# Kernel tuning notes

Measured on AMD Instinct MI355X. Metric: run time of the kernel, lower is better.

The kernel has to match this reference:

```python
import jax, jax.numpy as jnp
import numpy as np

B, T, D, H, L = 64, 512, 1024, 1024, 4


def setup_inputs() -> dict:
    key = jax.random.key(0)
    ks = jax.random.split(key, 5)
    scale = 1.0 / np.sqrt(H)
    return {
        "x": jax.random.normal(ks[0], (B, T, D), dtype=jnp.float32),
        "Wih": jax.random.normal(ks[1], (L, 4 * H, D), dtype=jnp.float32) * scale,
        "Whh": jax.random.normal(ks[2], (L, 4 * H, H), dtype=jnp.float32) * scale,
        "bih": jax.random.normal(ks[3], (L, 4 * H), dtype=jnp.float32) * scale,
        "bhh": jax.random.normal(ks[4], (L, 4 * H), dtype=jnp.float32) * scale,
    }


def _lstm_layer(x_tbd, Wih, Whh, b):
    # x_tbd: [T, B, in]; Wih: [4H, in]; Whh: [4H, H]; b: [4H]
    Bsz = x_tbd.shape[1]
    Hsz = Whh.shape[1]
    # precompute the input-side GEMM for the whole sequence in one shot
    xg = jnp.einsum('tbd,gd->tbg', x_tbd, Wih) + b  # [T, B, 4H]

    def step(carry, xg_t):
        h, c = carry
        z = xg_t + h @ Whh.T  # [B, 4H]
        i, f, g, o = jnp.split(z, 4, axis=-1)  # torch LSTMCell gate order
        c = jax.nn.sigmoid(f) * c + jax.nn.sigmoid(i) * jnp.tanh(g)
        h = jax.nn.sigmoid(o) * jnp.tanh(c)
        return (h, c), h

    init = (jnp.zeros((Bsz, Hsz), x_tbd.dtype), jnp.zeros((Bsz, Hsz), x_tbd.dtype))
    (h_last, _), hs = jax.lax.scan(step, init, xg)
    return hs, h_last  # hs: [T, B, H]


def reference(x, Wih, Whh, bih, bhh):
    # layer-by-layer over the stack (fixed small L); each layer scans over time
    seq = jnp.transpose(x, (1, 0, 2))  # [T, B, D]
    h_last = None
    for l in range(L):
        seq, h_last = _lstm_layer(seq, Wih[l], Whh[l], bih[l] + bhh[l])
    return h_last  # [B, output_size], hidden of last layer at final timestep
```

## Files before the change

### kernel.cpp

```cpp
#include <hip/hip_runtime.h>
#include <math.h>


#define BSZ 64
#define TSZ 512
#define DSZ 1024
#define HSZ 1024
#define LSZ 4
#define NBLK 256
#define NTHR 512
#define NSTEP (TSZ + LSZ - 1)
#define BUFB 32768

typedef _Float16 half8  __attribute__((ext_vector_type(8)));
typedef _Float16 half4  __attribute__((ext_vector_type(4)));
typedef _Float16 half2v __attribute__((ext_vector_type(2)));
typedef float    f32x4  __attribute__((ext_vector_type(4)));
typedef float    f32x8  __attribute__((ext_vector_type(8)));

constexpr size_t N_X  = (size_t)BSZ * TSZ * DSZ;
constexpr size_t N_H  = (size_t)2 * LSZ * BSZ * HSZ;
constexpr size_t OFF_X     = 0;
constexpr size_t OFF_H     = OFF_X + N_X * 2;
constexpr size_t OFF_FLAGS = OFF_H + N_H * 2;
constexpr size_t OFF_GEN   = OFF_FLAGS + (size_t)NBLK * 64;
constexpr size_t BAR_BYTES = (size_t)NBLK * 64 + 64;

__device__ inline float fsig(float x) {
  return __builtin_amdgcn_rcpf(1.0f + __expf(-x));
}
__device__ inline float ftanh(float x) {
  float e = __expf(fminf(2.0f * x, 80.0f));
  return 1.0f - 2.0f * __builtin_amdgcn_rcpf(e + 1.0f);
}

__device__ inline void gload16(const void* g, void* l) {
  __builtin_amdgcn_global_load_lds(
      (const __attribute__((address_space(1))) void*)g,
      (__attribute__((address_space(3))) void*)l, 16, 0, 0);
}

__device__ inline void gbar(unsigned* flags, unsigned* gen, unsigned tgt) {
  __syncthreads();
  if (blockIdx.x == 0) {
    const int t = threadIdx.x;
    if (t >= 1 && t < NBLK) {
      while (__hip_atomic_load(&flags[t * 16], __ATOMIC_RELAXED,
                               __HIP_MEMORY_SCOPE_AGENT) < tgt)
        __builtin_amdgcn_s_sleep(2);
    }
    __syncthreads();
    if (t == 0) {
      __hip_atomic_store(gen, tgt, __ATOMIC_RELAXED, __HIP_MEMORY_SCOPE_AGENT);
      __builtin_amdgcn_fence(__ATOMIC_ACQUIRE, "agent");
    }
  } else {
    if (threadIdx.x == 0) {
      __hip_atomic_store(&flags[(size_t)blockIdx.x * 16], tgt, __ATOMIC_RELAXED,
                         __HIP_MEMORY_SCOPE_AGENT);
      while (__hip_atomic_load(gen, __ATOMIC_RELAXED,
                               __HIP_MEMORY_SCOPE_AGENT) < tgt)
        __builtin_amdgcn_s_sleep(2);
      __builtin_amdgcn_fence(__ATOMIC_ACQUIRE, "agent");
    }
  }
  __syncthreads();
}

__global__ __launch_bounds__(NTHR, 1) void lstm_persistent(
    const float* __restrict__ xin, const float* __restrict__ Wih,
    const float* __restrict__ Whh, const float* __restrict__ bih,
    const float* __restrict__ bhh, float* __restrict__ out,
    char* __restrict__ ws)
{
  _Float16* x16   = (_Float16*)(ws + OFF_X);
  _Float16* h16   = (_Float16*)(ws + OFF_H);
  unsigned* flags = (unsigned*)(ws + OFF_FLAGS);
  unsigned* gen   = (unsigned*)(ws + OFF_GEN);

  const int tid  = threadIdx.x;
  const int gtid = blockIdx.x * NTHR + tid;
  const int lane = tid & 63;
  const int w    = tid >> 6;
  const int mat  = w >> 2;
  const int rp   = (w >> 1) & 1;
  const int kh   = w & 1;
  const int ln15 = lane & 15;
  const int lq   = lane >> 4;

  const int l  = blockIdx.x >> 6;
  const int cc = blockIdx.x & 63;
  const int c0 = cc * 16;

  const float* Wsel = mat ? Whh : Wih;
  half8 bw[2][16];
#pragma unroll
  for (int gl = 0; gl < 2; ++gl) {
    const float* wrow =
        Wsel + (size_t)(l * 4096 + (rp * 2 + gl) * 1024 + c0 + ln15) * 1024 +
        kh * 512;
#pragma unroll
    for (int ks = 0; ks < 16; ++ks) {
      f32x8 f = *(const f32x8*)(wrow + ks * 32 + lq * 8);
      bw[gl][ks] = __builtin_convertvector(f, half8);
    }
  }

  const int gb = tid >> 3;
  const int gc = (tid & 7) * 2;
  float bsg[4][2];
#pragma unroll
  for (int g = 0; g < 4; ++g) {
    const int bb = l * 4096 + g * 1024 + c0 + gc;
    bsg[g][0] = bih[bb] + bhh[bb];
    bsg[g][1] = bih[bb + 1] + bhh[bb + 1];
  }
  float cr0 = 0.f, cr1 = 0.f;

  const int sb   = tid >> 3;
  const int pswl = ((tid & 7) ^ (sb & 7)) << 4;
  const int dstb = (tid >> 6) << 10;

  {
    const f32x4* s4 = (const f32x4*)xin;
    unsigned long long* xu = (unsigned long long*)x16;
    const int dq = DSZ / 4;
    for (int i = gtid; i < (int)(N_X / 4); i += NBLK * NTHR) {
      const int d4  = i & (dq - 1);
      const int rem = i >> 8;
      const int tt  = rem & (TSZ - 1);
      const int bb  = rem >> 9;
      half4 v = __builtin_convertvector(s4[i], half4);
      const size_t o = ((size_t)tt * BSZ + bb) * dq + d4;
      __hip_atomic_store(&xu[o], __builtin_bit_cast(unsigned long long, v),
                         __ATOMIC_RELAXED, __HIP_MEMORY_SCOPE_AGENT);
    }
    unsigned long long* hz = (unsigned long long*)h16;
    for (int i = gtid; i < (int)(N_H / 4); i += NBLK * NTHR)
      __hip_atomic_store(&hz[i], 0ull, __ATOMIC_RELAXED,
                         __HIP_MEMORY_SCOPE_AGENT);
  }
  unsigned btgt = 1;
  gbar(flags, gen, btgt++);

  __shared__ __align__(16) char smem[3 * BUFB];
  float* pl = (float*)smem;

  const int lm1 = (l > 0) ? (l - 1) : 0;

  for (int s = 0; s < NSTEP; ++s) {
    const int t = s - l;
    if (t >= 0 && t < TSZ) {
      const int prevslot = (s + 1) & 1;
      const _Float16* hin  = h16 + (size_t)prevslot * (LSZ * BSZ * HSZ) +
                             (size_t)lm1 * (BSZ * HSZ);
      const _Float16* hown = h16 + (size_t)prevslot * (LSZ * BSZ * HSZ) +
                             (size_t)l * (BSZ * HSZ);
      const _Float16* base0 = (l == 0) ? x16 + (size_t)t * (BSZ * DSZ) : hin;

      const char* p0 = (const char*)(base0 + (size_t)sb * 1024) + pswl;
      const char* p1 = (const char*)(hown + (size_t)sb * HSZ) + pswl;

      auto stage = [&](int kc, int bsel) {
        const char* r0 = p0 + kc * 128;
        const char* r1 = p1 + kc * 128;
        char* d = smem + bsel * BUFB + dstb;
        gload16(r0,        d);
        gload16(r0 + 1024, d + 8192);
        gload16(r1,        d + 16384);
        gload16(r1 + 1024, d + 24576);
      };

      f32x4 acc[4][2] = {};

      stage(0, 0);
      stage(1, 1);
      __builtin_amdgcn_sched_barrier(0);
      asm volatile("s_waitcnt vmcnt(4)" ::: "memory");
      __builtin_amdgcn_s_barrier();
      __builtin_amdgcn_sched_barrier(0);

      const int rdoff = mat * 16384 + kh * 8192;
#pragma unroll
      for (int kc = 0; kc < 8; ++kc) {
        if (kc + 2 < 8) stage(kc + 2, (kc + 2) % 3);
        const char* rdb = smem + (kc % 3) * BUFB + rdoff;
#pragma unroll
        for (int ksl = 0; ksl < 2; ++ksl) {
#pragma unroll
          for (int mt = 0; mt < 4; ++mt) {
            const int row = mt * 16 + ln15;
            const half8 a = *(const half8*)(rdb + row * 128 +
                                            ((ksl * 64 + lq * 16) ^
                                             ((row & 7) << 4)));
            acc[mt][0] = __builtin_amdgcn_mfma_f32_16x16x32_f16(
                a, bw[0][kc * 2 + ksl], acc[mt][0], 0, 0, 0);
            acc[mt][1] = __builtin_amdgcn_mfma_f32_16x16x32_f16(
                a, bw[1][kc * 2 + ksl], acc[mt][1], 0, 0, 0);
          }
        }
        __builtin_amdgcn_sched_barrier(0);
        if (kc <= 5)      asm volatile("s_waitcnt vmcnt(4)" ::: "memory");
        else if (kc == 6) asm volatile("s_waitcnt vmcnt(0)" ::: "memory");
        __builtin_amdgcn_s_barrier();
        __builtin_amdgcn_sched_barrier(0);
      }

      if (l == 0 && t + 1 < TSZ) {
        const char* xnext =
            (const char*)(x16 + (size_t)(t + 1) * (BSZ * DSZ)) +
            ((cc >> 3) & 7) * 16384;
        char* trash = smem + 2 * BUFB + dstb;
        gload16(xnext + tid * 16, trash);
        gload16(xnext + 8192 + tid * 16, trash);
      }

      {
        const int pbase = (mat * 2 + kh) * 4096;
#pragma unroll
        for (int mt = 0; mt < 4; ++mt)
#pragma unroll
          for (int gl = 0; gl < 2; ++gl) {
            const int v  = (rp * 2 + gl) * 16 + ln15;
            const int bp = (mt * 16 + lq * 4) ^ ((ln15 & 7) << 2);
            *(f32x4*)&pl[pbase + v * 64 + bp] = acc[mt][gl];
          }
      }
      __builtin_amdgcn_sched_barrier(0);
      asm volatile("s_waitcnt lgkmcnt(0)" ::: "memory");
      __builtin_amdgcn_s_barrier();
      __builtin_amdgcn_sched_barrier(0);

      {
        float z[4][2];
#pragma unroll
        for (int g = 0; g < 4; ++g)
#pragma unroll
          for (int j = 0; j < 2; ++j) {
            const int v  = g * 16 + gc + j;
            const int bp = gb ^ ((v & 7) << 2);
            z[g][j] = pl[0 * 4096 + v * 64 + bp] +
                      pl[1 * 4096 + v * 64 + bp] +
                      pl[2 * 4096 + v * 64 + bp] +
                      pl[3 * 4096 + v * 64 + bp] + bsg[g][j];
          }
        float cn0 = fsig(z[1][0]) * cr0 + fsig(z[0][0]) * ftanh(z[2][0]);
        float cn1 = fsig(z[1][1]) * cr1 + fsig(z[0][1]) * ftanh(z[2][1]);
        float hn0 = fsig(z[3][0]) * ftanh(cn0);
        float hn1 = fsig(z[3][1]) * ftanh(cn1);
        cr0 = cn0; cr1 = cn1;
        half2v hv; hv[0] = (_Float16)hn0; hv[1] = (_Float16)hn1;
        const size_t ho = (size_t)(s & 1) * (LSZ * BSZ * HSZ) +
                          (size_t)l * (BSZ * HSZ) + (size_t)gb * HSZ + c0 + gc;
        __hip_atomic_store((unsigned*)(h16 + ho),
                           __builtin_bit_cast(unsigned, hv),
                           __ATOMIC_RELAXED, __HIP_MEMORY_SCOPE_AGENT);
        if (l == LSZ - 1 && t == TSZ - 1) {
          out[(size_t)gb * HSZ + c0 + gc]     = hn0;
          out[(size_t)gb * HSZ + c0 + gc + 1] = hn1;
        }
      }
    }
    gbar(flags, gen, btgt++);
  }
}

extern "C" void kernel_launch(void* const* d_in, const int* in_sizes, int n_in,
                              void* d_out, int out_size, void* d_ws, size_t ws_size,
                              hipStream_t stream) {
  const float* x   = (const float*)d_in[0];
  const float* Wih = (const float*)d_in[1];
  const float* Whh = (const float*)d_in[2];
  const float* bih = (const float*)d_in[3];
  const float* bhh = (const float*)d_in[4];
  float* out = (float*)d_out;
  char*  ws  = (char*)d_ws;

  hipMemsetAsync(ws + OFF_FLAGS, 0, BAR_BYTES, stream);

  void* args[] = {(void*)&x, (void*)&Wih, (void*)&Whh, (void*)&bih,
                  (void*)&bhh, (void*)&out, (void*)&ws};
  hipLaunchCooperativeKernel((const void*)lstm_persistent, dim3(NBLK), dim3(NTHR),
                             args, 0, stream);
}
```

Baseline: 4.563 ms.

## Split K across four waves per matrix and drop x-prefetch warm loads

Each wave now covers all four gates but only a quarter of the K range, instead of two gates over half of K. Each A fragment loaded from LDS is then reused across four MFMAs rather than two, which halves LDS reads per MFMA. The cost is a larger partial-sum buffer: eight partials per output instead of four, so shared memory grows to four buffers and the reduction does more LDS reads. The speculative L2 warm-up loads of the next timestep's x for layer 0 are also removed.

Result: slower. 4.901 ms (+7.4%).

```diff
diff --git a/kernel.cpp b/kernel.cpp
--- a/kernel.cpp
+++ b/kernel.cpp
@@ -83,8 +83,7 @@
   const int lane = tid & 63;
   const int w    = tid >> 6;
   const int mat  = w >> 2;
-  const int rp   = (w >> 1) & 1;
-  const int kh   = w & 1;
+  const int kq   = w & 3;
   const int ln15 = lane & 15;
   const int lq   = lane >> 4;
 
@@ -93,16 +92,16 @@
   const int c0 = cc * 16;
 
   const float* Wsel = mat ? Whh : Wih;
-  half8 bw[2][16];
-#pragma unroll
-  for (int gl = 0; gl < 2; ++gl) {
+  half8 bw[4][8];
+#pragma unroll
+  for (int g = 0; g < 4; ++g) {
     const float* wrow =
-        Wsel + (size_t)(l * 4096 + (rp * 2 + gl) * 1024 + c0 + ln15) * 1024 +
-        kh * 512;
-#pragma unroll
-    for (int ks = 0; ks < 16; ++ks) {
-      f32x8 f = *(const f32x8*)(wrow + ks * 32 + lq * 8);
-      bw[gl][ks] = __builtin_convertvector(f, half8);
+        Wsel + (size_t)(l * 4096 + g * 1024 + c0 + ln15) * 1024 +
+        (kq >> 1) * 512 + (kq & 1) * 32 + lq * 8;
+#pragma unroll
+    for (int kc = 0; kc < 8; ++kc) {
+      f32x8 f = *(const f32x8*)(wrow + kc * 64);
+      bw[g][kc] = __builtin_convertvector(f, half8);
     }
   }
 
@@ -143,7 +142,7 @@
   unsigned btgt = 1;
   gbar(flags, gen, btgt++);
 
-  __shared__ __align__(16) char smem[3 * BUFB];
+  __shared__ __align__(16) char smem[4 * BUFB];
   float* pl = (float*)smem;
 
   const int lm1 = (l > 0) ? (l - 1) : 0;
@@ -171,7 +170,7 @@
         gload16(r1 + 1024, d + 24576);
       };
 
-      f32x4 acc[4][2] = {};
+      f32x4 acc[4][4] = {};
 
       stage(0, 0);
       stage(1, 1);
@@ -180,25 +179,25 @@
       __builtin_amdgcn_s_barrier();
       __builtin_amdgcn_sched_barrier(0);
 
-      const int rdoff = mat * 16384 + kh * 8192;
+      const int rdoff = mat * 16384 + (kq >> 1) * 8192;
+      const int rdo   = (kq & 1) * 64 + lq * 16;
 #pragma unroll
       for (int kc = 0; kc < 8; ++kc) {
         if (kc + 2 < 8) stage(kc + 2, (kc + 2) % 3);
         const char* rdb = smem + (kc % 3) * BUFB + rdoff;
-#pragma unroll
-        for (int ksl = 0; ksl < 2; ++ksl) {
-#pragma unroll
-          for (int mt = 0; mt < 4; ++mt) {
-            const int row = mt * 16 + ln15;
-            const half8 a = *(const half8*)(rdb + row * 128 +
-                                            ((ksl * 64 + lq * 16) ^
-                                             ((row & 7) << 4)));
-            acc[mt][0] = __builtin_amdgcn_mfma_f32_16x16x32_f16(
-                a, bw[0][kc * 2 + ksl], acc[mt][0], 0, 0, 0);
-            acc[mt][1] = __builtin_amdgcn_mfma_f32_16x16x32_f16(
-                a, bw[1][kc * 2 + ksl], acc[mt][1], 0, 0, 0);
-          }
+        half8 a[4];
+#pragma unroll
+        for (int mt = 0; mt < 4; ++mt) {
+          const int row = mt * 16 + ln15;
+          a[mt] = *(const half8*)(rdb + row * 128 +
+                                  (rdo ^ ((row & 7) << 4)));
         }
+#pragma unroll
+        for (int g = 0; g < 4; ++g)
+#pragma unroll
+          for (int mt = 0; mt < 4; ++mt)
+            acc[mt][g] = __builtin_amdgcn_mfma_f32_16x16x32_f16(
+                a[mt], bw[g][kc], acc[mt][g], 0, 0, 0);
         __builtin_amdgcn_sched_barrier(0);
         if (kc <= 5)      asm volatile("s_waitcnt vmcnt(4)" ::: "memory");
         else if (kc == 6) asm volatile("s_waitcnt vmcnt(0)" ::: "memory");
@@ -206,24 +205,15 @@
         __builtin_amdgcn_sched_barrier(0);
       }
 
-      if (l == 0 && t + 1 < TSZ) {
-        const char* xnext =
-            (const char*)(x16 + (size_t)(t + 1) * (BSZ * DSZ)) +
-            ((cc >> 3) & 7) * 16384;
-        char* trash = smem + 2 * BUFB + dstb;
-        gload16(xnext + tid * 16, trash);
-        gload16(xnext + 8192 + tid * 16, trash);
-      }
-
       {
-        const int pbase = (mat * 2 + kh) * 4096;
+        const int pbase = w * 4096;
 #pragma unroll
         for (int mt = 0; mt < 4; ++mt)
 #pragma unroll
-          for (int gl = 0; gl < 2; ++gl) {
-            const int v  = (rp * 2 + gl) * 16 + ln15;
+          for (int g = 0; g < 4; ++g) {
+            const int v  = g * 16 + ln15;
             const int bp = (mt * 16 + lq * 4) ^ ((ln15 & 7) << 2);
-            *(f32x4*)&pl[pbase + v * 64 + bp] = acc[mt][gl];
+            *(f32x4*)&pl[pbase + v * 64 + bp] = acc[mt][g];
           }
       }
       __builtin_amdgcn_sched_barrier(0);
@@ -239,10 +229,11 @@
           for (int j = 0; j < 2; ++j) {
             const int v  = g * 16 + gc + j;
             const int bp = gb ^ ((v & 7) << 2);
-            z[g][j] = pl[0 * 4096 + v * 64 + bp] +
-                      pl[1 * 4096 + v * 64 + bp] +
-                      pl[2 * 4096 + v * 64 + bp] +
-                      pl[3 * 4096 + v * 64 + bp] + bsg[g][j];
+            float sum = 0.f;
+#pragma unroll
+            for (int p = 0; p < 8; ++p)
+              sum += pl[p * 4096 + v * 64 + bp];
+            z[g][j] = sum + bsg[g][j];
           }
         float cn0 = fsig(z[1][0]) * cr0 + fsig(z[0][0]) * ftanh(z[2][0]);
         float cn1 = fsig(z[1][1]) * cr1 + fsig(z[0][1]) * ftanh(z[2][1]);
```

## Switch to double-buffered 64KB LDS stages with wider K chunks per barrier

Applied to the files above, without the earlier changes.

The K loop of the recurrent step now runs in 4 chunks of 256 K each, double-buffered in two 64KB LDS buffers, in place of 8 chunks of 128 triple-buffered in 32KB buffers. The global-to-LDS load mapping and swizzle are rebuilt so each thread loads 16-byte pieces into contiguous destination slots. The layer-0 prefetch of the next timestep's x into a scratch buffer is removed. This halves the number of block barriers per step, but each wait now drains all outstanding loads (vmcnt(0)), which may expose more load latency. LDS use grows from 96KB to 128KB.

Result: slower. 4.743 ms (+4.0%).

```diff
diff --git a/kernel.cpp b/kernel.cpp
--- a/kernel.cpp
+++ b/kernel.cpp
@@ -10,7 +10,7 @@
 #define NBLK 256
 #define NTHR 512
 #define NSTEP (TSZ + LSZ - 1)
-#define BUFB 32768
+#define BUFB 65536
 
 typedef _Float16 half8  __attribute__((ext_vector_type(8)));
 typedef _Float16 half4  __attribute__((ext_vector_type(4)));
@@ -117,9 +117,9 @@
   }
   float cr0 = 0.f, cr1 = 0.f;
 
-  const int sb   = tid >> 3;
-  const int pswl = ((tid & 7) ^ (sb & 7)) << 4;
-  const int dstb = (tid >> 6) << 10;
+  const int bA   = w * 4 + (lane >> 4);
+  const int slg  = (((ln15 & 8) | ((ln15 & 7) ^ (bA & 7)))) << 4;
+  const int dstb = tid * 16;
 
   {
     const f32x4* s4 = (const f32x4*)xin;
@@ -143,7 +143,7 @@
   unsigned btgt = 1;
   gbar(flags, gen, btgt++);
 
-  __shared__ __align__(16) char smem[3 * BUFB];
+  __shared__ __align__(16) char smem[2 * BUFB];
   float* pl = (float*)smem;
 
   const int lm1 = (l > 0) ? (l - 1) : 0;
@@ -158,61 +158,57 @@
                              (size_t)l * (BSZ * HSZ);
       const _Float16* base0 = (l == 0) ? x16 + (size_t)t * (BSZ * DSZ) : hin;
 
-      const char* p0 = (const char*)(base0 + (size_t)sb * 1024) + pswl;
-      const char* p1 = (const char*)(hown + (size_t)sb * HSZ) + pswl;
+      const char* q0A = (const char*)(base0 + (size_t)bA * 1024) + slg;
+      const char* q0B = q0A + 32 * 2048;
+      const char* q1A = (const char*)(hown + (size_t)bA * 1024) + slg;
+      const char* q1B = q1A + 32 * 2048;
 
       auto stage = [&](int kc, int bsel) {
-        const char* r0 = p0 + kc * 128;
-        const char* r1 = p1 + kc * 128;
+        const int kb = kc * 256;
         char* d = smem + bsel * BUFB + dstb;
-        gload16(r0,        d);
-        gload16(r0 + 1024, d + 8192);
-        gload16(r1,        d + 16384);
-        gload16(r1 + 1024, d + 24576);
+        gload16(q0A + kb,        d);
+        gload16(q0B + kb,        d + 8192);
+        gload16(q0A + 1024 + kb, d + 16384);
+        gload16(q0B + 1024 + kb, d + 24576);
+        gload16(q1A + kb,        d + 32768);
+        gload16(q1B + kb,        d + 40960);
+        gload16(q1A + 1024 + kb, d + 49152);
+        gload16(q1B + 1024 + kb, d + 57344);
       };
 
       f32x4 acc[4][2] = {};
 
       stage(0, 0);
-      stage(1, 1);
-      __builtin_amdgcn_sched_barrier(0);
-      asm volatile("s_waitcnt vmcnt(4)" ::: "memory");
+      __builtin_amdgcn_sched_barrier(0);
+      asm volatile("s_waitcnt vmcnt(0)" ::: "memory");
       __builtin_amdgcn_s_barrier();
       __builtin_amdgcn_sched_barrier(0);
 
-      const int rdoff = mat * 16384 + kh * 8192;
-#pragma unroll
-      for (int kc = 0; kc < 8; ++kc) {
-        if (kc + 2 < 8) stage(kc + 2, (kc + 2) % 3);
-        const char* rdb = smem + (kc % 3) * BUFB + rdoff;
-#pragma unroll
-        for (int ksl = 0; ksl < 2; ++ksl) {
+      const int rdoff = mat * 32768 + kh * 16384;
+#pragma unroll
+      for (int kc = 0; kc < 4; ++kc) {
+        if (kc < 3) stage(kc + 1, (kc + 1) & 1);
+        const char* rdb = smem + (kc & 1) * BUFB + rdoff;
+#pragma unroll
+        for (int ksl = 0; ksl < 4; ++ksl) {
 #pragma unroll
           for (int mt = 0; mt < 4; ++mt) {
             const int row = mt * 16 + ln15;
-            const half8 a = *(const half8*)(rdb + row * 128 +
+            const half8 a = *(const half8*)(rdb + row * 256 +
                                             ((ksl * 64 + lq * 16) ^
                                              ((row & 7) << 4)));
             acc[mt][0] = __builtin_amdgcn_mfma_f32_16x16x32_f16(
-                a, bw[0][kc * 2 + ksl], acc[mt][0], 0, 0, 0);
+                a, bw[0][kc * 4 + ksl], acc[mt][0], 0, 0, 0);
             acc[mt][1] = __builtin_amdgcn_mfma_f32_16x16x32_f16(
-                a, bw[1][kc * 2 + ksl], acc[mt][1], 0, 0, 0);
+                a, bw[1][kc * 4 + ksl], acc[mt][1], 0, 0, 0);
           }
         }
-        __builtin_amdgcn_sched_barrier(0);
-        if (kc <= 5)      asm volatile("s_waitcnt vmcnt(4)" ::: "memory");
-        else if (kc == 6) asm volatile("s_waitcnt vmcnt(0)" ::: "memory");
-        __builtin_amdgcn_s_barrier();
-        __builtin_amdgcn_sched_barrier(0);
-      }
-
-      if (l == 0 && t + 1 < TSZ) {
-        const char* xnext =
-            (const char*)(x16 + (size_t)(t + 1) * (BSZ * DSZ)) +
-            ((cc >> 3) & 7) * 16384;
-        char* trash = smem + 2 * BUFB + dstb;
-        gload16(xnext + tid * 16, trash);
-        gload16(xnext + 8192 + tid * 16, trash);
+        if (kc < 3) {
+          __builtin_amdgcn_sched_barrier(0);
+          asm volatile("s_waitcnt vmcnt(0)" ::: "memory");
+          __builtin_amdgcn_s_barrier();
+          __builtin_amdgcn_sched_barrier(0);
+        }
       }
 
       {
```

## Replace per-step grid barrier with layer-local dataflow flags and triple-buffered h

Applied to the files above, without the earlier changes.

Swaps the global grid barrier run after every wavefront step for per-block progress flags. Each block waits only on its own layer, the layer below for the current step, and the layer above for the previous step. The hidden-state buffer grows from two to three slots so a block running ahead cannot overwrite data a slower neighbour layer still reads. This aims to cut the serialising cost of a 256-block barrier each step and let layers drift, at the price of more flag polling and extra workspace.

Result: faster. 4.221 ms (-7.5%).

```diff
diff --git a/kernel.cpp b/kernel.cpp
--- a/kernel.cpp
+++ b/kernel.cpp
@@ -19,12 +19,14 @@
 typedef float    f32x8  __attribute__((ext_vector_type(8)));
 
 constexpr size_t N_X  = (size_t)BSZ * TSZ * DSZ;
-constexpr size_t N_H  = (size_t)2 * LSZ * BSZ * HSZ;
+constexpr size_t N_H  = (size_t)3 * LSZ * BSZ * HSZ;
+constexpr size_t HSLOT = (size_t)LSZ * BSZ * HSZ;
 constexpr size_t OFF_X     = 0;
 constexpr size_t OFF_H     = OFF_X + N_X * 2;
 constexpr size_t OFF_FLAGS = OFF_H + N_H * 2;
 constexpr size_t OFF_GEN   = OFF_FLAGS + (size_t)NBLK * 64;
-constexpr size_t BAR_BYTES = (size_t)NBLK * 64 + 64;
+constexpr size_t OFF_DF    = OFF_GEN + 64;
+constexpr size_t BAR_BYTES = (size_t)NBLK * 64 + 64 + (size_t)NBLK * 64;
 
 __device__ inline float fsig(float x) {
   return __builtin_amdgcn_rcpf(1.0f + __expf(-x));
@@ -65,6 +67,39 @@
     }
   }
   __syncthreads();
+}
+
+__device__ inline void dwait(unsigned* df, int l, unsigned s) {
+  const int t = threadIdx.x;
+  if (t < 64) {
+    while (__hip_atomic_load(&df[(size_t)(l * 64 + t) * 16], __ATOMIC_RELAXED,
+                             __HIP_MEMORY_SCOPE_AGENT) < s)
+      __builtin_amdgcn_s_sleep(2);
+  } else if (t < 128) {
+    if (l > 0) {
+      while (__hip_atomic_load(&df[(size_t)((l - 1) * 64 + (t - 64)) * 16],
+                               __ATOMIC_RELAXED,
+                               __HIP_MEMORY_SCOPE_AGENT) < s)
+        __builtin_amdgcn_s_sleep(2);
+    }
+  } else if (t < 192) {
+    if (l < LSZ - 1 && s > 0) {
+      while (__hip_atomic_load(&df[(size_t)((l + 1) * 64 + (t - 128)) * 16],
+                               __ATOMIC_RELAXED,
+                               __HIP_MEMORY_SCOPE_AGENT) < s - 1)
+        __builtin_amdgcn_s_sleep(2);
+    }
+  }
+  __syncthreads();
+  if (t == 0) __builtin_amdgcn_fence(__ATOMIC_ACQUIRE, "agent");
+  __syncthreads();
+}
+
+__device__ inline void dpost(unsigned* df, unsigned cnt) {
+  __syncthreads();
+  if (threadIdx.x == 0)
+    __hip_atomic_store(&df[(size_t)blockIdx.x * 16], cnt, __ATOMIC_RELAXED,
+                       __HIP_MEMORY_SCOPE_AGENT);
 }
 
 __global__ __launch_bounds__(NTHR, 1) void lstm_persistent(
@@ -77,6 +112,7 @@
   _Float16* h16   = (_Float16*)(ws + OFF_H);
   unsigned* flags = (unsigned*)(ws + OFF_FLAGS);
   unsigned* gen   = (unsigned*)(ws + OFF_GEN);
+  unsigned* df    = (unsigned*)(ws + OFF_DF);
 
   const int tid  = threadIdx.x;
   const int gtid = blockIdx.x * NTHR + tid;
@@ -140,21 +176,23 @@
       __hip_atomic_store(&hz[i], 0ull, __ATOMIC_RELAXED,
                          __HIP_MEMORY_SCOPE_AGENT);
   }
-  unsigned btgt = 1;
-  gbar(flags, gen, btgt++);
+  gbar(flags, gen, 1u);
 
   __shared__ __align__(16) char smem[3 * BUFB];
   float* pl = (float*)smem;
 
   const int lm1 = (l > 0) ? (l - 1) : 0;
+  int wslot = 0;
 
   for (int s = 0; s < NSTEP; ++s) {
+    dwait(df, l, (unsigned)s);
+
     const int t = s - l;
     if (t >= 0 && t < TSZ) {
-      const int prevslot = (s + 1) & 1;
-      const _Float16* hin  = h16 + (size_t)prevslot * (LSZ * BSZ * HSZ) +
+      const int rslot = (wslot + 2) % 3;
+      const _Float16* hin  = h16 + (size_t)rslot * HSLOT +
                              (size_t)lm1 * (BSZ * HSZ);
-      const _Float16* hown = h16 + (size_t)prevslot * (LSZ * BSZ * HSZ) +
+      const _Float16* hown = h16 + (size_t)rslot * HSLOT +
                              (size_t)l * (BSZ * HSZ);
       const _Float16* base0 = (l == 0) ? x16 + (size_t)t * (BSZ * DSZ) : hin;
 
@@ -250,8 +288,8 @@
         float hn1 = fsig(z[3][1]) * ftanh(cn1);
         cr0 = cn0; cr1 = cn1;
         half2v hv; hv[0] = (_Float16)hn0; hv[1] = (_Float16)hn1;
-        const size_t ho = (size_t)(s & 1) * (LSZ * BSZ * HSZ) +
-                          (size_t)l * (BSZ * HSZ) + (size_t)gb * HSZ + c0 + gc;
+        const size_t ho = (size_t)wslot * HSLOT + (size_t)l * (BSZ * HSZ) +
+                          (size_t)gb * HSZ + c0 + gc;
         __hip_atomic_store((unsigned*)(h16 + ho),
                            __builtin_bit_cast(unsigned, hv),
                            __ATOMIC_RELAXED, __HIP_MEMORY_SCOPE_AGENT);
@@ -261,7 +299,9 @@
         }
       }
     }
-    gbar(flags, gen, btgt++);
+
+    dpost(df, (unsigned)(s + 1));
+    wslot = (wslot == 2) ? 0 : wslot + 1;
   }
 }
 
```
